# Performance work log

Hardware: AMD Instinct MI355X
Metric: run time of the kernel (lower is better)

The kernel has to match this reference:

```python
import jax, jax.numpy as jnp
import numpy as np

N_EMBD = 1024
N_HEAD = 16
B, T, T_MEM = 4, 1024, 1024


def setup_inputs() -> dict:
    key = jax.random.key(0)
    ks = jax.random.split(key, 11)
    s = 1.0 / np.sqrt(N_EMBD)
    return {
        "q_in": jax.random.normal(ks[0], (B, T, N_EMBD), jnp.float32),
        "k_in": jax.random.normal(ks[1], (B, T_MEM, N_EMBD), jnp.float32),
        "v_in": jax.random.normal(ks[2], (B, T_MEM, N_EMBD), jnp.float32),
        # torch nn.Linear weights: [out_features, in_features]
        "Wq": jax.random.normal(ks[3], (N_EMBD, N_EMBD), jnp.float32) * s,
        "bq": jax.random.normal(ks[4], (N_EMBD,), jnp.float32) * s,
        "Wk": jax.random.normal(ks[5], (N_EMBD, N_EMBD), jnp.float32) * s,
        "bk": jax.random.normal(ks[6], (N_EMBD,), jnp.float32) * s,
        "Wv": jax.random.normal(ks[7], (N_EMBD, N_EMBD), jnp.float32) * s,
        "bv": jax.random.normal(ks[8], (N_EMBD,), jnp.float32) * s,
        "Wo": jax.random.normal(ks[9], (N_EMBD, N_EMBD), jnp.float32) * s,
        "bo": jax.random.normal(ks[10], (N_EMBD,), jnp.float32) * s,
    }


def reference(q_in, k_in, v_in, Wq, bq, Wk, bk, Wv, bv, Wo, bo):
    b, t, c = q_in.shape
    t_mem = k_in.shape[1]
    hd = c // N_HEAD  # head dim

    def proj(x, W, bias):
        return x @ W.T + bias

    # [b, h, t, hd]
    q = proj(q_in, Wq, bq).reshape(b, t, N_HEAD, hd).transpose(0, 2, 1, 3)
    k = proj(k_in, Wk, bk).reshape(b, t_mem, N_HEAD, hd).transpose(0, 2, 1, 3)
    v = proj(v_in, Wv, bv).reshape(b, t_mem, N_HEAD, hd).transpose(0, 2, 1, 3)

    scale = 1.0 / np.sqrt(hd).astype(np.float32)
    att = jnp.einsum("bhqd,bhkd->bhqk", q, k) * scale
    att = jax.nn.softmax(att, axis=-1)  # dropout p=0 -> identity

    y = jnp.einsum("bhqk,bhkd->bhqd", att, v)
    y = y.transpose(0, 2, 1, 3).reshape(b, t, c)
    y = proj(y, Wo, bo)  # resid_drop p=0 -> identity

    attention = jnp.mean(att, axis=1)  # mean over heads: [b, t, t_mem]
    return (y, attention)
```

## Files before the change

kernel.cpp:

```cpp
#include <hip/hip_runtime.h>
#include <hip/hip_fp16.h>


typedef __attribute__((ext_vector_type(8))) short s16x8;
typedef __attribute__((ext_vector_type(4))) float f32x4;
typedef __attribute__((ext_vector_type(4))) unsigned short u16x4;

#define N_EMBD 1024
#define NH 16
#define BT 4096
#define STR 1032

#if __has_builtin(__builtin_amdgcn_global_load_lds)
#define HAVE_GLL 1
#define GLDS16(g, l)                                                              \
  __builtin_amdgcn_global_load_lds((__attribute__((address_space(1))) void*)(g), \
                                   (__attribute__((address_space(3))) void*)(l), 16, 0, 0)
#else
#define HAVE_GLL 0
#endif

static __device__ __forceinline__ unsigned short f2bf(float f) {
  unsigned int u = __builtin_bit_cast(unsigned int, f);
  u += 0x7FFFu + ((u >> 16) & 1u);
  return (unsigned short)(u >> 16);
}
static __device__ __forceinline__ float bf2f(unsigned short h) {
  return __builtin_bit_cast(float, ((unsigned int)h) << 16);
}

__global__ __launch_bounds__(256) void cvt_in3(const float* __restrict__ q,
                                               const float* __restrict__ k,
                                               const float* __restrict__ v,
                                               unsigned short* __restrict__ out) {
  const int z = blockIdx.z;
  const float* src = (z == 0) ? q : (z == 1 ? k : v);
  int i = (blockIdx.x * 256 + threadIdx.x) * 4;
  float4 val = *(const float4*)(src + i);
  u16x4 o;
  o[0] = f2bf(val.x);
  o[1] = f2bf(val.y);
  o[2] = f2bf(val.z);
  o[3] = f2bf(val.w);
  *(u16x4*)(out + (size_t)z * BT * N_EMBD + i) = o;
}

__global__ __launch_bounds__(256) void cvt_w4(const float* __restrict__ wo,
                                              const float* __restrict__ wq,
                                              const float* __restrict__ wk,
                                              const float* __restrict__ wv,
                                              unsigned short* __restrict__ out) {
  const int z = blockIdx.z;
  const float* src = (z == 0) ? wo : (z == 1 ? wq : (z == 2 ? wk : wv));
  const float scale = (z == 1) ? 0.125f : 1.0f;
  int i = (blockIdx.x * 256 + threadIdx.x) * 4;
  float4 val = *(const float4*)(src + i);
  u16x4 o;
  o[0] = f2bf(val.x * scale);
  o[1] = f2bf(val.y * scale);
  o[2] = f2bf(val.z * scale);
  o[3] = f2bf(val.w * scale);
  *(u16x4*)(out + (size_t)z * N_EMBD * N_EMBD + i) = o;
}

template <bool F32OUT>
static __device__ __forceinline__ void gemm_bt_tile(const unsigned short* __restrict__ A,
                                                    const unsigned short* __restrict__ B,
                                                    const float* __restrict__ bias, float bscale,
                                                    void* __restrict__ Cout,
                                                    int m0, int n0, int N, int K,
                                                    unsigned short* Al, unsigned short* Bl) {
  const int tid = threadIdx.x;
  const int l = tid & 63, w = tid >> 6;
  const int wr = w >> 1, wc = w & 1;
  const int l15 = l & 15, l4 = l >> 4;
  const int srow = tid >> 3;
  const int skk = (tid & 7) * 8;
  f32x4 acc[4][4] = {};
  for (int k0 = 0; k0 < K; k0 += 64) {
#if HAVE_GLL
#pragma unroll
    for (int i = 0; i < 4; ++i) {
      GLDS16(&A[(size_t)(m0 + i * 32 + srow) * K + k0 + skk], Al + i * 2048 + w * 512);
      GLDS16(&B[(size_t)(n0 + i * 32 + srow) * K + k0 + skk], Bl + i * 2048 + w * 512);
    }
#else
#pragma unroll
    for (int i = 0; i < 4; ++i) {
      int row = i * 32 + srow;
      *(s16x8*)&Al[row * 64 + skk] = *(const s16x8*)&A[(size_t)(m0 + row) * K + k0 + skk];
      *(s16x8*)&Bl[row * 64 + skk] = *(const s16x8*)&B[(size_t)(n0 + row) * K + k0 + skk];
    }
#endif
    __syncthreads();
#pragma unroll
    for (int kf = 0; kf < 2; ++kf) {
      s16x8 af[4], bfr[4];
#pragma unroll
      for (int mi = 0; mi < 4; ++mi)
        af[mi] = *(const s16x8*)&Al[(wr * 64 + mi * 16 + l15) * 64 + kf * 32 + l4 * 8];
#pragma unroll
      for (int nj = 0; nj < 4; ++nj)
        bfr[nj] = *(const s16x8*)&Bl[(wc * 64 + nj * 16 + l15) * 64 + kf * 32 + l4 * 8];
#pragma unroll
      for (int mi = 0; mi < 4; ++mi) {
#pragma unroll
        for (int nj = 0; nj < 4; ++nj)
          acc[mi][nj] =
              __builtin_amdgcn_mfma_f32_16x16x32_bf16(af[mi], bfr[nj], acc[mi][nj], 0, 0, 0);
      }
    }
    __syncthreads();
  }
#pragma unroll
  for (int nj = 0; nj < 4; ++nj) {
    int col = n0 + wc * 64 + nj * 16 + l15;
    float bv = bias[col] * bscale;
#pragma unroll
    for (int mi = 0; mi < 4; ++mi) {
#pragma unroll
      for (int r = 0; r < 4; ++r) {
        int row = m0 + wr * 64 + mi * 16 + l4 * 4 + r;
        float v = acc[mi][nj][r] + bv;
        if constexpr (F32OUT)
          ((float*)Cout)[(size_t)row * N + col] = v;
        else
          ((unsigned short*)Cout)[(size_t)row * N + col] = f2bf(v);
      }
    }
  }
}

__global__ __launch_bounds__(256) void gemm_qkv(const unsigned short* __restrict__ Xin,
                                                const unsigned short* __restrict__ Wbf,
                                                const float* __restrict__ bq,
                                                const float* __restrict__ bk,
                                                const float* __restrict__ bv,
                                                unsigned short* __restrict__ Cout) {
  __shared__ unsigned short Al[128 * 64];
  __shared__ unsigned short Bl[128 * 64];
  const int z = blockIdx.z;
  const float* bias = (z == 0) ? bq : (z == 1 ? bk : bv);
  const float bscale = (z == 0) ? 0.125f : 1.0f;
  gemm_bt_tile<false>(Xin + (size_t)z * BT * N_EMBD,
                      Wbf + (size_t)(1 + z) * N_EMBD * N_EMBD, bias, bscale,
                      Cout + (size_t)z * BT * N_EMBD, blockIdx.x * 128, blockIdx.y * 128,
                      N_EMBD, N_EMBD, Al, Bl);
}

__global__ __launch_bounds__(256) void gemm_out(const unsigned short* __restrict__ Ybf,
                                                const unsigned short* __restrict__ Wo,
                                                const float* __restrict__ bo,
                                                float* __restrict__ Cout) {
  __shared__ unsigned short Al[128 * 64];
  __shared__ unsigned short Bl[128 * 64];
  gemm_bt_tile<true>(Ybf, Wo, bo, 1.0f, Cout, blockIdx.x * 128, blockIdx.y * 128, N_EMBD, N_EMBD,
                     Al, Bl);
}

__global__ __launch_bounds__(256) void transpose_v(const unsigned short* __restrict__ Vp,
                                                   unsigned short* __restrict__ Vt) {
  __shared__ unsigned short tile[64][65];
  const int t0 = blockIdx.x * 64, h = blockIdx.y, b = blockIdx.z;
  const int r = threadIdx.x >> 2, c0 = (threadIdx.x & 3) * 16;
  const unsigned short* src = Vp + (size_t)(b * 1024 + t0 + r) * 1024 + h * 64 + c0;
#pragma unroll
  for (int j = 0; j < 16; ++j) tile[r][c0 + j] = src[j];
  __syncthreads();
  unsigned short* dst = Vt + (size_t)((b * 16 + h) * 64 + r) * 1024 + t0 + c0;
#pragma unroll
  for (int j = 0; j < 16; ++j) dst[j] = tile[c0 + j][r];
}

__global__ __launch_bounds__(512, 4) void attn_ph2(const unsigned short* __restrict__ Qp,
                                                   const unsigned short* __restrict__ Kp,
                                                   const unsigned short* __restrict__ Vt,
                                                   unsigned short* __restrict__ Ybf,
                                                   unsigned short* __restrict__ Pmean) {
  __shared__ __align__(16) unsigned short S2[2][16 * STR];
  __shared__ float RedM[2][16][4];
  __shared__ float RedS[2][16][4];
  const int tid = threadIdx.x;
  const int tm = tid >> 8;
  const int ttid = tid & 255;
  const int w4 = ttid >> 6;
  const int l = tid & 63;
  const int l15 = l & 15, l4 = l >> 4;
  const int r = ttid & 15, c = ttid >> 4;

  int bid = blockIdx.x;
  int swz = (bid & 7) * 64 + (bid >> 3);
  int qt = swz & 63;
  int grp = swz >> 6;
  int b = grp >> 1, hg = grp & 1;
  int q0 = qt * 16;

  __half2 am[32];
#pragma unroll
  for (int j = 0; j < 32; ++j) am[j] = __float2half2_rn(0.f);

#pragma unroll 1
  for (int it = 0; it < 4; ++it) {
    const int h = hg * 8 + it * 2 + tm;
    const unsigned short* qbase = Qp + (size_t)(b * 1024 + q0 + l15) * 1024 + h * 64 + l4 * 8;
    s16x8 aq0 = *(const s16x8*)qbase;
    s16x8 aq1 = *(const s16x8*)(qbase + 32);
#pragma unroll
    for (int nt = 0; nt < 16; ++nt) {
      int gn = w4 * 16 + nt;
      const unsigned short* kb = Kp + (size_t)(b * 1024 + gn * 16 + l15) * 1024 + h * 64 + l4 * 8;
      f32x4 sacc = {};
      sacc = __builtin_amdgcn_mfma_f32_16x16x32_bf16(aq0, *(const s16x8*)kb, sacc, 0, 0, 0);
      sacc = __builtin_amdgcn_mfma_f32_16x16x32_bf16(aq1, *(const s16x8*)(kb + 32), sacc, 0, 0, 0);
#pragma unroll
      for (int rr = 0; rr < 4; ++rr)
        S2[tm][(l4 * 4 + rr) * STR + gn * 16 + l15] = f2bf(sacc[rr]);
    }
    __syncthreads();

    float m = -3.4e38f;
#pragma unroll
    for (int k = 0; k < 8; ++k) {
      s16x8 sv = *(const s16x8*)&S2[tm][r * STR + c * 16 + (k >> 1) * 256 + (k & 1) * 8];
#pragma unroll
      for (int j = 0; j < 8; ++j) m = fmaxf(m, bf2f((unsigned short)sv[j]));
    }
    m = fmaxf(m, __shfl_xor(m, 16));
    m = fmaxf(m, __shfl_xor(m, 32));
    if (l < 16) RedM[tm][l][w4] = m;
    __syncthreads();

    float mm = fmaxf(fmaxf(RedM[tm][r][0], RedM[tm][r][1]),
                     fmaxf(RedM[tm][r][2], RedM[tm][r][3]));
    float ps = 0.f;
#pragma unroll
    for (int k = 0; k < 8; ++k) {
      unsigned short* sp = &S2[tm][r * STR + c * 16 + (k >> 1) * 256 + (k & 1) * 8];
      s16x8 sv = *(const s16x8*)sp;
      s16x8 pv;
#pragma unroll
      for (int j = 0; j < 8; ++j) {
        float e = __expf(bf2f((unsigned short)sv[j]) - mm);
        ps += e;
        pv[j] = (short)f2bf(e);
      }
      *(s16x8*)sp = pv;
    }
    ps += __shfl_xor(ps, 16);
    ps += __shfl_xor(ps, 32);
    if (l < 16) RedS[tm][l][w4] = ps;
    __syncthreads();

    float lsA = RedS[tm][l15][0] + RedS[tm][l15][1] + RedS[tm][l15][2] + RedS[tm][l15][3];
    float fac = 0.0625f / lsA;
    f32x4 y = {};
    const unsigned short* vb = Vt + (size_t)((b * 16 + h) * 64 + w4 * 16 + l15) * 1024 + l4 * 8;
#pragma unroll
    for (int kq = 0; kq < 4; ++kq) {
#pragma unroll
      for (int kk = 0; kk < 8; ++kk) {
        const int ks = kq * 8 + kk;
        s16x8 pa = *(const s16x8*)&S2[tm][l15 * STR + ks * 32 + l4 * 8];
        y = __builtin_amdgcn_mfma_f32_16x16x32_bf16(pa, *(const s16x8*)(vb + ks * 32), y, 0, 0, 0);
        if (kq == w4) {
#pragma unroll
          for (int e2 = 0; e2 < 4; ++e2) {
            float2 fv;
            fv.x = bf2f((unsigned short)pa[e2 * 2]) * fac;
            fv.y = bf2f((unsigned short)pa[e2 * 2 + 1]) * fac;
            am[kk * 4 + e2] = __hadd2(am[kk * 4 + e2], __float22half2_rn(fv));
          }
        }
      }
    }
#pragma unroll
    for (int rr = 0; rr < 4; ++rr) {
      int row = l4 * 4 + rr;
      float lsr = RedS[tm][row][0] + RedS[tm][row][1] + RedS[tm][row][2] + RedS[tm][row][3];
      Ybf[(size_t)(b * 1024 + q0 + row) * 1024 + h * 64 + w4 * 16 + l15] = f2bf(y[rr] / lsr);
    }
    __syncthreads();
  }

  unsigned int* us = (unsigned int*)S2;
  if (tm == 1) {
#pragma unroll
    for (int j = 0; j < 32; ++j) us[ttid * 32 + j] = __builtin_bit_cast(unsigned int, am[j]);
  }
  __syncthreads();
  if (tm == 0) {
    unsigned short* pm =
        Pmean + (size_t)((b * 2 + hg) * 1024 + q0 + l15) * 1024 + w4 * 256 + l4 * 8;
#pragma unroll
    for (int kk = 0; kk < 8; ++kk) {
      s16x8 ov;
#pragma unroll
      for (int e2 = 0; e2 < 4; ++e2) {
        int j = kk * 4 + e2;
        __half2 ot = __builtin_bit_cast(__half2, us[ttid * 32 + j]);
        float2 fo = __half22float2(ot);
        float2 fm = __half22float2(am[j]);
        ov[e2 * 2] = (short)f2bf(fm.x + fo.x);
        ov[e2 * 2 + 1] = (short)f2bf(fm.y + fo.y);
      }
      *(s16x8*)&pm[kk * 32] = ov;
    }
  }
}

__global__ __launch_bounds__(256) void mean2(const unsigned short* __restrict__ P2,
                                             float* __restrict__ out) {
  size_t f = ((size_t)blockIdx.x * 256 + threadIdx.x) * 8;
  int b = (int)(f >> 20);
  size_t i0 = f + ((size_t)b << 20);
  s16x8 a = *(const s16x8*)&P2[i0];
  s16x8 d = *(const s16x8*)&P2[i0 + (1u << 20)];
  float4 o0, o1;
  o0.x = bf2f((unsigned short)a[0]) + bf2f((unsigned short)d[0]);
  o0.y = bf2f((unsigned short)a[1]) + bf2f((unsigned short)d[1]);
  o0.z = bf2f((unsigned short)a[2]) + bf2f((unsigned short)d[2]);
  o0.w = bf2f((unsigned short)a[3]) + bf2f((unsigned short)d[3]);
  o1.x = bf2f((unsigned short)a[4]) + bf2f((unsigned short)d[4]);
  o1.y = bf2f((unsigned short)a[5]) + bf2f((unsigned short)d[5]);
  o1.z = bf2f((unsigned short)a[6]) + bf2f((unsigned short)d[6]);
  o1.w = bf2f((unsigned short)a[7]) + bf2f((unsigned short)d[7]);
  *(float4*)&out[f] = o0;
  *(float4*)&out[f + 4] = o1;
}

extern "C" void kernel_launch(void* const* d_in, const int* in_sizes, int n_in, void* d_out,
                              int out_size, void* d_ws, size_t ws_size, hipStream_t stream) {
  const float* q_in = (const float*)d_in[0];
  const float* k_in = (const float*)d_in[1];
  const float* v_in = (const float*)d_in[2];
  const float* Wq = (const float*)d_in[3];
  const float* bq = (const float*)d_in[4];
  const float* Wk = (const float*)d_in[5];
  const float* bk = (const float*)d_in[6];
  const float* Wv = (const float*)d_in[7];
  const float* bv = (const float*)d_in[8];
  const float* Wo = (const float*)d_in[9];
  const float* bo = (const float*)d_in[10];

  float* out_y = (float*)d_out;
  float* out_att = out_y + (size_t)BT * N_EMBD;

  char* ws = (char*)d_ws;
  const size_t MB = 1024 * 1024;
  unsigned short* xin_bf = (unsigned short*)(ws);
  unsigned short* W_bf = (unsigned short*)(ws + 24 * MB);
  unsigned short* Qp = (unsigned short*)(ws + 32 * MB);
  unsigned short* Kp = Qp + (size_t)BT * N_EMBD;
  unsigned short* Vp = Kp + (size_t)BT * N_EMBD;
  unsigned short* Pmean = (unsigned short*)(ws);
  unsigned short* Vt = (unsigned short*)(ws + 16 * MB);
  unsigned short* Ybf = Vp;

  const int NIN = BT * N_EMBD;
  const int NW = N_EMBD * N_EMBD;

  cvt_in3<<<dim3(NIN / 1024, 1, 3), 256, 0, stream>>>(q_in, k_in, v_in, xin_bf);
  cvt_w4<<<dim3(NW / 1024, 1, 4), 256, 0, stream>>>(Wo, Wq, Wk, Wv, W_bf);

  gemm_qkv<<<dim3(BT / 128, N_EMBD / 128, 3), 256, 0, stream>>>(xin_bf, W_bf, bq, bk, bv, Qp);
  transpose_v<<<dim3(16, 16, 4), 256, 0, stream>>>(Vp, Vt);
  attn_ph2<<<512, 512, 0, stream>>>(Qp, Kp, Vt, Ybf, Pmean);
  mean2<<<2048, 256, 0, stream>>>(Pmean, out_att);
  gemm_out<<<dim3(BT / 128, N_EMBD / 128), 256, 0, stream>>>(Ybf, W_bf, bo, out_y);
}
```

Baseline: 235.5 us.

## Keep attention scores in registers for softmax, write normalized probabilities once

The QK^T MFMA operands are swapped so each lane holds a transposed score tile. Max, exp and sum now run on the fp32 accumulators in registers instead of storing bf16 scores to LDS and reading them back twice. Probabilities are normalized before a single LDS store, and the head-mean accumulation comes from registers, which removes the per-row divide in the output store. This saves LDS traffic and one barrier phase, and rounds to bf16 only once. The cost is 64 extra accumulator registers per lane, which may reduce occupancy.

Result: slower. 267.9 us (+13.8%).

```diff
diff --git a/kernel.cpp b/kernel.cpp
--- a/kernel.cpp
+++ b/kernel.cpp
@@ -186,7 +186,6 @@
   const int w4 = ttid >> 6;
   const int l = tid & 63;
   const int l15 = l & 15, l4 = l >> 4;
-  const int r = ttid & 15, c = ttid >> 4;
 
   int bid = blockIdx.x;
   int swz = (bid & 7) * 64 + (bid >> 3);
@@ -205,79 +204,67 @@
     const unsigned short* qbase = Qp + (size_t)(b * 1024 + q0 + l15) * 1024 + h * 64 + l4 * 8;
     s16x8 aq0 = *(const s16x8*)qbase;
     s16x8 aq1 = *(const s16x8*)(qbase + 32);
+    f32x4 sacc[16];
 #pragma unroll
     for (int nt = 0; nt < 16; ++nt) {
       int gn = w4 * 16 + nt;
       const unsigned short* kb = Kp + (size_t)(b * 1024 + gn * 16 + l15) * 1024 + h * 64 + l4 * 8;
-      f32x4 sacc = {};
-      sacc = __builtin_amdgcn_mfma_f32_16x16x32_bf16(aq0, *(const s16x8*)kb, sacc, 0, 0, 0);
-      sacc = __builtin_amdgcn_mfma_f32_16x16x32_bf16(aq1, *(const s16x8*)(kb + 32), sacc, 0, 0, 0);
-#pragma unroll
-      for (int rr = 0; rr < 4; ++rr)
-        S2[tm][(l4 * 4 + rr) * STR + gn * 16 + l15] = f2bf(sacc[rr]);
-    }
-    __syncthreads();
-
+      f32x4 s = {};
+      s = __builtin_amdgcn_mfma_f32_16x16x32_bf16(*(const s16x8*)kb, aq0, s, 0, 0, 0);
+      s = __builtin_amdgcn_mfma_f32_16x16x32_bf16(*(const s16x8*)(kb + 32), aq1, s, 0, 0, 0);
+      sacc[nt] = s;
+    }
     float m = -3.4e38f;
 #pragma unroll
-    for (int k = 0; k < 8; ++k) {
-      s16x8 sv = *(const s16x8*)&S2[tm][r * STR + c * 16 + (k >> 1) * 256 + (k & 1) * 8];
-#pragma unroll
-      for (int j = 0; j < 8; ++j) m = fmaxf(m, bf2f((unsigned short)sv[j]));
-    }
+    for (int nt = 0; nt < 16; ++nt)
+#pragma unroll
+      for (int rr = 0; rr < 4; ++rr) m = fmaxf(m, sacc[nt][rr]);
     m = fmaxf(m, __shfl_xor(m, 16));
     m = fmaxf(m, __shfl_xor(m, 32));
     if (l < 16) RedM[tm][l][w4] = m;
     __syncthreads();
-
-    float mm = fmaxf(fmaxf(RedM[tm][r][0], RedM[tm][r][1]),
-                     fmaxf(RedM[tm][r][2], RedM[tm][r][3]));
+    float mm = fmaxf(fmaxf(RedM[tm][l15][0], RedM[tm][l15][1]),
+                     fmaxf(RedM[tm][l15][2], RedM[tm][l15][3]));
     float ps = 0.f;
 #pragma unroll
-    for (int k = 0; k < 8; ++k) {
-      unsigned short* sp = &S2[tm][r * STR + c * 16 + (k >> 1) * 256 + (k & 1) * 8];
-      s16x8 sv = *(const s16x8*)sp;
-      s16x8 pv;
-#pragma unroll
-      for (int j = 0; j < 8; ++j) {
-        float e = __expf(bf2f((unsigned short)sv[j]) - mm);
+    for (int nt = 0; nt < 16; ++nt)
+#pragma unroll
+      for (int rr = 0; rr < 4; ++rr) {
+        float e = __expf(sacc[nt][rr] - mm);
+        sacc[nt][rr] = e;
         ps += e;
-        pv[j] = (short)f2bf(e);
       }
-      *(s16x8*)sp = pv;
-    }
     ps += __shfl_xor(ps, 16);
     ps += __shfl_xor(ps, 32);
     if (l < 16) RedS[tm][l][w4] = ps;
     __syncthreads();
-
-    float lsA = RedS[tm][l15][0] + RedS[tm][l15][1] + RedS[tm][l15][2] + RedS[tm][l15][3];
-    float fac = 0.0625f / lsA;
+    float tot = RedS[tm][l15][0] + RedS[tm][l15][1] + RedS[tm][l15][2] + RedS[tm][l15][3];
+    float inv = 1.0f / tot;
+    float fac = inv * 0.0625f;
+#pragma unroll
+    for (int nt = 0; nt < 16; ++nt) {
+      u16x4 pk;
+#pragma unroll
+      for (int rr = 0; rr < 4; ++rr) pk[rr] = f2bf(sacc[nt][rr] * inv);
+      *(u16x4*)&S2[tm][l15 * STR + (w4 * 16 + nt) * 16 + l4 * 4] = pk;
+      float2 f0 = make_float2(sacc[nt][0] * fac, sacc[nt][1] * fac);
+      float2 f1 = make_float2(sacc[nt][2] * fac, sacc[nt][3] * fac);
+      am[nt * 2] = __hadd2(am[nt * 2], __float22half2_rn(f0));
+      am[nt * 2 + 1] = __hadd2(am[nt * 2 + 1], __float22half2_rn(f1));
+    }
+    __syncthreads();
+
     f32x4 y = {};
     const unsigned short* vb = Vt + (size_t)((b * 16 + h) * 64 + w4 * 16 + l15) * 1024 + l4 * 8;
 #pragma unroll
-    for (int kq = 0; kq < 4; ++kq) {
-#pragma unroll
-      for (int kk = 0; kk < 8; ++kk) {
-        const int ks = kq * 8 + kk;
-        s16x8 pa = *(const s16x8*)&S2[tm][l15 * STR + ks * 32 + l4 * 8];
-        y = __builtin_amdgcn_mfma_f32_16x16x32_bf16(pa, *(const s16x8*)(vb + ks * 32), y, 0, 0, 0);
-        if (kq == w4) {
-#pragma unroll
-          for (int e2 = 0; e2 < 4; ++e2) {
-            float2 fv;
-            fv.x = bf2f((unsigned short)pa[e2 * 2]) * fac;
-            fv.y = bf2f((unsigned short)pa[e2 * 2 + 1]) * fac;
-            am[kk * 4 + e2] = __hadd2(am[kk * 4 + e2], __float22half2_rn(fv));
-          }
-        }
-      }
+    for (int ks = 0; ks < 32; ++ks) {
+      s16x8 pa = *(const s16x8*)&S2[tm][l15 * STR + ks * 32 + l4 * 8];
+      y = __builtin_amdgcn_mfma_f32_16x16x32_bf16(pa, *(const s16x8*)(vb + ks * 32), y, 0, 0, 0);
     }
 #pragma unroll
     for (int rr = 0; rr < 4; ++rr) {
       int row = l4 * 4 + rr;
-      float lsr = RedS[tm][row][0] + RedS[tm][row][1] + RedS[tm][row][2] + RedS[tm][row][3];
-      Ybf[(size_t)(b * 1024 + q0 + row) * 1024 + h * 64 + w4 * 16 + l15] = f2bf(y[rr] / lsr);
+      Ybf[(size_t)(b * 1024 + q0 + row) * 1024 + h * 64 + w4 * 16 + l15] = f2bf(y[rr]);
     }
     __syncthreads();
   }
@@ -290,20 +277,20 @@
   __syncthreads();
   if (tm == 0) {
     unsigned short* pm =
-        Pmean + (size_t)((b * 2 + hg) * 1024 + q0 + l15) * 1024 + w4 * 256 + l4 * 8;
-#pragma unroll
-    for (int kk = 0; kk < 8; ++kk) {
-      s16x8 ov;
-#pragma unroll
-      for (int e2 = 0; e2 < 4; ++e2) {
-        int j = kk * 4 + e2;
+        Pmean + (size_t)((b * 2 + hg) * 1024 + q0 + l15) * 1024 + w4 * 256 + l4 * 4;
+#pragma unroll
+    for (int nt = 0; nt < 16; ++nt) {
+      u16x4 ov;
+#pragma unroll
+      for (int p = 0; p < 2; ++p) {
+        int j = nt * 2 + p;
         __half2 ot = __builtin_bit_cast(__half2, us[ttid * 32 + j]);
         float2 fo = __half22float2(ot);
         float2 fm = __half22float2(am[j]);
-        ov[e2 * 2] = (short)f2bf(fm.x + fo.x);
-        ov[e2 * 2 + 1] = (short)f2bf(fm.y + fo.y);
+        ov[p * 2] = f2bf(fm.x + fo.x);
+        ov[p * 2 + 1] = f2bf(fm.y + fo.y);
       }
-      *(s16x8*)&pm[kk * 32] = ov;
+      *(u16x4*)&pm[nt * 16] = ov;
     }
   }
 }
```
